# Kernel tuning notes

Hardware: AMD Instinct MI355X
Metric: run time of the kernel (lower is better)

Reference implementation:

```python
import jax, jax.numpy as jnp
import numpy as np

B, S = 512, 200            # batch, max_seq_len
D = H = 512                # embedding_dim must equal hidden_dim (ht init from embedded input)
VOCAB, USERS, SKILLS, OUT = 2002, 10000, 1001, 1001


def setup_inputs() -> dict:
    key = jax.random.key(0)
    ks = jax.random.split(key, 15)
    s = 0.05
    enc_emb = jax.random.normal(ks[0], (VOCAB, D)) * s
    enc_emb = enc_emb.at[0].set(0.0)  # padding_idx=0
    P = jax.random.normal(ks[1], (USERS, H)) * s
    Q = jax.random.normal(ks[2], (SKILLS, H)) * s
    P_bias = jax.random.normal(ks[3], (USERS, 1)) * s
    Q_bias = jax.random.normal(ks[4], (SKILLS, 1)) * s
    W_ih = jax.random.normal(ks[5], (4 * H, D)) * s   # torch LSTMCell weight_ih
    W_hh = jax.random.normal(ks[6], (4 * H, H)) * s   # torch LSTMCell weight_hh
    b_ih = jax.random.normal(ks[7], (4 * H,)) * s
    b_hh = jax.random.normal(ks[8], (4 * H,)) * s
    dec_W = jax.random.normal(ks[9], (OUT, H)) * s    # nn.Linear weight
    dec_b = jax.random.normal(ks[10], (OUT,)) * s
    main_input = jax.random.randint(ks[11], (B, S), 0, VOCAB)
    target_id = jax.random.randint(ks[12], (B, 1), 0, OUT)
    user_id_sequence = jax.random.randint(ks[13], (B, S), 0, USERS)
    skill_id_sequence = jax.random.randint(ks[14], (B, S), 0, SKILLS)
    return dict(main_input=main_input, target_id=target_id,
                user_id_sequence=user_id_sequence, skill_id_sequence=skill_id_sequence,
                enc_emb=enc_emb, P=P, Q=Q, P_bias=P_bias, Q_bias=Q_bias,
                W_ih=W_ih, W_hh=W_hh, b_ih=b_ih, b_hh=b_hh, dec_W=dec_W, dec_b=dec_b)


def reference(main_input, target_id, user_id_sequence, skill_id_sequence,
              enc_emb, P, Q, P_bias, Q_bias, W_ih, W_hh, b_ih, b_hh, dec_W, dec_b):
    x = enc_emb[main_input]                                    # [B,S,D] (dropout in eval mode = identity)
    # MF extended input: sigmoid(sum(P*Q, dim=2, keepdim) + P_bias + Q_bias) -> [B,S,1]
    mf = jax.nn.sigmoid(jnp.sum(P[user_id_sequence] * Q[skill_id_sequence], axis=2, keepdims=True)
                        + P_bias[user_id_sequence] + Q_bias[skill_id_sequence])

    def step(carry, inp):
        ht, ct = carry
        xt, et = inp                                           # xt:[B,D], et:[B,1]
        ct = ct + ct * et                                      # custom gating before cell update
        gates = xt @ W_ih.T + b_ih + ht @ W_hh.T + b_hh        # [B,4H], torch gate order i,f,g,o
        i, f, g, o = jnp.split(gates, 4, axis=-1)
        ct = jax.nn.sigmoid(f) * ct + jax.nn.sigmoid(i) * jnp.tanh(g)
        ht = jax.nn.sigmoid(o) * jnp.tanh(ct)
        return (ht, ct), None

    h0 = jnp.zeros((x.shape[0], H), x.dtype)
    (ht, _), _ = jax.lax.scan(step, (h0, h0),
                              (jnp.swapaxes(x, 0, 1), jnp.swapaxes(mf, 0, 1)))
    out = ht @ dec_W.T + dec_b                                 # [B,OUT]
    out = jnp.take_along_axis(out, target_id, axis=-1)         # [B,1]
    return jax.nn.sigmoid(out)
```

## Files before the change

kernel.cpp:

```cpp
#include <hip/hip_runtime.h>

typedef __attribute__((ext_vector_type(8))) short short8;
typedef __attribute__((ext_vector_type(4))) float floatx4;
typedef __attribute__((ext_vector_type(16))) float floatx16;
typedef unsigned int uint;
typedef unsigned short ushort;
typedef unsigned long long ull;
typedef __attribute__((ext_vector_type(4))) uint uintx4;
typedef __attribute__((ext_vector_type(4))) int intx4;

#define B_ 512
#define S_ 200
#define H_ 512
#define VOCAB_ 2002

__device__ __forceinline__ ushort f2bfbits(float f) {
  union { float f; uint u; } c; c.f = f;
  uint u = c.u;
  u += 0x7fffu + ((u >> 16) & 1u);
  return (ushort)(u >> 16);
}
__device__ __forceinline__ float bf2f_(ushort u) {
  union { uint i; float f; } c; c.i = ((uint)u) << 16; return c.f;
}
__device__ __forceinline__ float sigmoidf_(float x) { return 1.f / (1.f + __expf(-x)); }
__device__ __forceinline__ float tanhf_(float x) { return 2.f / (1.f + __expf(-2.f * x)) - 1.f; }
__device__ __forceinline__ float clamp30(float x) { return fminf(fmaxf(x, -30.f), 30.f); }

__device__ __forceinline__ void split8(const float* p, short8& hi, short8& lo) {
#pragma unroll
  for (int j = 0; j < 8; ++j) {
    const float f = p[j];
    const ushort h = f2bfbits(f);
    hi[j] = (short)h;
    lo[j] = (short)f2bfbits(f - bf2f_(h));
  }
}

__device__ __forceinline__ void ld16_cc(const void* p, uintx4& a) {
  asm volatile("global_load_dwordx4 %0, %1, off sc0 sc1"
               : "=&v"(a)
               : "v"(p));
}
__device__ __forceinline__ int ld4_cc_wait(const int* p) {
  int v;
  asm volatile("global_load_dword %0, %1, off sc0 sc1\n\t"
               "s_waitcnt vmcnt(0)"
               : "=v"(v)
               : "v"(p)
               : "memory");
  return v;
}
__device__ __forceinline__ void vm_wait0() {
  asm volatile("s_waitcnt vmcnt(0)" ::: "memory");
}
__device__ __forceinline__ void vm_wait4() {
  asm volatile("s_waitcnt vmcnt(4)" ::: "memory");
}

template <typename ET>
__global__ void encg_kernel(const float* __restrict__ emb, const float* __restrict__ Wih,
                            ET* __restrict__ encg) {
  const int w = threadIdx.x >> 6, l = threadIdx.x & 63;
  const int ln = l & 15, lk = l >> 4;
  const int n = (blockIdx.x * 4 + w) * 16 + ln;
  const int m = blockIdx.y * 16 + ln;
  const int mA = (m < VOCAB_) ? m : 0;
  const float* ap = emb + (size_t)mA * 512 + lk * 8;
  const float* bp = Wih + (size_t)n * 512 + lk * 8;
  floatx4 acc = {0.f, 0.f, 0.f, 0.f};
#pragma unroll 4
  for (int kk = 0; kk < 16; ++kk) {
    short8 ah, al, bh, bl;
    split8(ap + kk * 32, ah, al);
    split8(bp + kk * 32, bh, bl);
    acc = __builtin_amdgcn_mfma_f32_16x16x32_bf16(ah, bh, acc, 0, 0, 0);
    acc = __builtin_amdgcn_mfma_f32_16x16x32_bf16(ah, bl, acc, 0, 0, 0);
    acc = __builtin_amdgcn_mfma_f32_16x16x32_bf16(al, bh, acc, 0, 0, 0);
  }
#pragma unroll
  for (int r = 0; r < 4; ++r) {
    const int mo = blockIdx.y * 16 + lk * 4 + r;
    if (mo < VOCAB_) {
      if constexpr (sizeof(ET) == 2)
        encg[(size_t)mo * 2048 + n] = (ET)f2bfbits(acc[r]);
      else
        encg[(size_t)mo * 2048 + n] = acc[r];
    }
  }
}

__global__ void mf_kernel(const int* __restrict__ us, const int* __restrict__ ss,
                          const float* __restrict__ P, const float* __restrict__ Q,
                          const float* __restrict__ Pb, const float* __restrict__ Qb,
                          float* __restrict__ etb) {
  const int s = blockIdx.x;
  const int w = threadIdx.x >> 6, l = threadIdx.x & 63;
  const int b = blockIdx.y * 4 + w;
  const int u = us[b * S_ + s];
  const int k = ss[b * S_ + s];
  const float4 p0 = *(const float4*)(P + (size_t)u * 512 + l * 8);
  const float4 p1 = *(const float4*)(P + (size_t)u * 512 + l * 8 + 4);
  const float4 q0 = *(const float4*)(Q + (size_t)k * 512 + l * 8);
  const float4 q1 = *(const float4*)(Q + (size_t)k * 512 + l * 8 + 4);
  float dot = p0.x*q0.x + p0.y*q0.y + p0.z*q0.z + p0.w*q0.w
            + p1.x*q1.x + p1.y*q1.y + p1.z*q1.z + p1.w*q1.w;
#pragma unroll
  for (int off = 32; off > 0; off >>= 1) dot += __shfl_xor(dot, off);
  if (l == 0)
    etb[s * B_ + b] = sigmoidf_(dot + Pb[u] + Qb[k]);
}

template <typename ET>
__global__ __launch_bounds__(512, 2) void lstm_kernel(
    const int* __restrict__ tok, const ET* __restrict__ encg,
    const float* __restrict__ etb, const float* __restrict__ Whh,
    const float* __restrict__ bih, const float* __restrict__ bhh,
    ushort* ht_hi, ushort* ht_lo, int* ctr) {
  __shared__ __align__(16) ushort Ah_lds[32 * 512];
  __shared__ __align__(16) ushort Al_lds[32 * 512];
  __shared__ float gp_lds[2 * 128 * 33];

  const int bid = blockIdx.x;
  const int g = bid & 15, ns = bid >> 4;
  const int b0 = g * 32, h0 = ns * 32;
  const int tid = threadIdx.x;
  const int w = tid >> 6, l = tid & 63;
  const int nt = w & 3;
  const int kh = w >> 2;

  int* const myslot = ctr + g * 16 + ns;
  const int* const gslots = ctr + g * 16;

  short8 Bh[16], Bl[16];
  {
    const float* wr = Whh + (size_t)(nt * 512 + h0 + (l & 31)) * 512
                    + kh * 256 + (l >> 5) * 8;
#pragma unroll 4
    for (int kk = 0; kk < 16; ++kk)
      split8(wr + kk * 16, Bh[kk], Bl[kk]);
  }

  const int sr = tid >> 4;
  const int sc = tid & 15;
  const int hh = sc * 2;
  const int bg = b0 + sr;
  float ct0 = 0.f, ct1 = 0.f;

  float bs[4][2];
#pragma unroll
  for (int qq = 0; qq < 4; ++qq) {
    const int col = qq * 512 + h0 + hh;
    bs[qq][0] = bih[col] + bhh[col];
    bs[qq][1] = bih[col + 1] + bhh[col + 1];
  }

  const int swzw = (sr & 7) << 3;
  const int swzr = (l & 7) << 3;
  const int k8 = (l >> 5) * 8;
  const int sc8 = sc * 8;

  auto mfma_half = [&](int base) -> floatx16 {
    floatx16 a = {0.f,0.f,0.f,0.f,0.f,0.f,0.f,0.f,
                  0.f,0.f,0.f,0.f,0.f,0.f,0.f,0.f};
#pragma unroll
    for (int kk = 0; kk < 16; ++kk) {
      const int ao = (l & 31) * 512 + ((base + kk * 16 + k8) ^ swzr);
      const short8 ah = *(const short8*)(Ah_lds + ao);
      const short8 al = *(const short8*)(Al_lds + ao);
      a = __builtin_amdgcn_mfma_f32_32x32x16_bf16(ah, Bh[kk], a, 0, 0, 0);
      a = __builtin_amdgcn_mfma_f32_32x32x16_bf16(ah, Bl[kk], a, 0, 0, 0);
      a = __builtin_amdgcn_mfma_f32_32x32x16_bf16(al, Bh[kk], a, 0, 0, 0);
    }
    return a;
  };
  auto gp_write = [&](const floatx16& a) {
    float* gpw = gp_lds + kh * 4224 + (nt * 32 + (l & 31)) * 33 + 4 * (l >> 5);
#pragma unroll
    for (int r = 0; r < 16; ++r)
      gpw[(r & 3) + 8 * (r >> 2)] = a[r];
  };

  for (int s = 0; s < S_; ++s) {
    const int tv = tok[bg * S_ + s];
    float ev = etb[s * B_ + bg];
    float ex[4], ey[4];
#pragma unroll
    for (int qq = 0; qq < 4; ++qq) {
      if constexpr (sizeof(ET) == 2) {
        const uint e2 = *(const uint*)((const ushort*)encg + (size_t)tv * 2048 + qq * 512 + h0 + hh);
        ex[qq] = bf2f_((ushort)(e2 & 0xffffu)); ey[qq] = bf2f_((ushort)(e2 >> 16));
      } else {
        const float2 e = *(const float2*)((const float*)encg + (size_t)tv * 2048 + qq * 512 + h0 + hh);
        ex[qq] = e.x; ey[qq] = e.y;
      }
    }

    if (s > 0 && tid < 16) {
      const int* sp = gslots + tid;
      while (ld4_cc_wait(sp) < s) {}
    }
    __syncthreads();

    const size_t rdo = (size_t)(s & 1) * (B_ * H_);
    const size_t wro = (size_t)((s & 1) ^ 1) * (B_ * H_);
    const ushort* hrow = ht_hi + rdo + (size_t)bg * 512;
    const ushort* lrow = ht_lo + rdo + (size_t)bg * 512;

    uintx4 a0, a1, b0_, b1_;
    uintx4 a2, a3, b2_, b3_;
    __builtin_amdgcn_sched_barrier(0);
    ld16_cc(hrow + sc8,       a0);
    ld16_cc(hrow + sc8 + 128, a1);
    ld16_cc(lrow + sc8,       b0_);
    ld16_cc(lrow + sc8 + 128, b1_);
    ld16_cc(hrow + sc8 + 256, a2);
    ld16_cc(hrow + sc8 + 384, a3);
    ld16_cc(lrow + sc8 + 256, b2_);
    ld16_cc(lrow + sc8 + 384, b3_);
    vm_wait4();
    __builtin_amdgcn_sched_barrier(0);
    {
      const int base = sr * 512;
      *(uintx4*)(Ah_lds + base + (sc8 ^ swzw))         = a0;
      *(uintx4*)(Ah_lds + base + ((sc8 + 128) ^ swzw)) = a1;
      *(uintx4*)(Al_lds + base + (sc8 ^ swzw))         = b0_;
      *(uintx4*)(Al_lds + base + ((sc8 + 128) ^ swzw)) = b1_;
    }
    __syncthreads();

    floatx16 acc;
    if (kh == 0) {
      acc = mfma_half(0);
      gp_write(acc);
      vm_wait0();
      __builtin_amdgcn_sched_barrier(0);
      const int base = sr * 512;
      *(uintx4*)(Ah_lds + base + ((sc8 + 256) ^ swzw)) = a2;
      *(uintx4*)(Ah_lds + base + ((sc8 + 384) ^ swzw)) = a3;
      *(uintx4*)(Al_lds + base + ((sc8 + 256) ^ swzw)) = b2_;
      *(uintx4*)(Al_lds + base + ((sc8 + 384) ^ swzw)) = b3_;
    } else {
      vm_wait0();
      __builtin_amdgcn_sched_barrier(0);
      const int base = sr * 512;
      *(uintx4*)(Ah_lds + base + ((sc8 + 256) ^ swzw)) = a2;
      *(uintx4*)(Ah_lds + base + ((sc8 + 384) ^ swzw)) = a3;
      *(uintx4*)(Al_lds + base + ((sc8 + 256) ^ swzw)) = b2_;
      *(uintx4*)(Al_lds + base + ((sc8 + 384) ^ swzw)) = b3_;
    }
    __syncthreads();

    if (kh == 1) {
      acc = mfma_half(256);
      gp_write(acc);
    }
    __syncthreads();

    {
      ev = fminf(fmaxf(ev, 0.f), 1.f);
      float Gv[4][2];
#pragma unroll
      for (int qq = 0; qq < 4; ++qq) {
        const int cb0 = (qq * 32 + hh) * 33 + sr;
        const int cb1 = (qq * 32 + hh + 1) * 33 + sr;
        Gv[qq][0] = clamp30(gp_lds[cb0] + gp_lds[4224 + cb0] + ex[qq] + bs[qq][0]);
        Gv[qq][1] = clamp30(gp_lds[cb1] + gp_lds[4224 + cb1] + ey[qq] + bs[qq][1]);
      }
      const float scale = 1.f + ev;
      float c0v = ct0 * scale;
      c0v = sigmoidf_(Gv[1][0]) * c0v + sigmoidf_(Gv[0][0]) * tanhf_(Gv[2][0]);
      const float h0v = sigmoidf_(Gv[3][0]) * tanhf_(c0v);
      ct0 = c0v;
      float c1v = ct1 * scale;
      c1v = sigmoidf_(Gv[1][1]) * c1v + sigmoidf_(Gv[0][1]) * tanhf_(Gv[2][1]);
      const float h1v = sigmoidf_(Gv[3][1]) * tanhf_(c1v);
      ct1 = c1v;
      const ushort h0h = f2bfbits(h0v), h1h = f2bfbits(h1v);
      const ushort h0l = f2bfbits(h0v - bf2f_(h0h)), h1l = f2bfbits(h1v - bf2f_(h1h));
      const size_t wo = wro + (size_t)bg * 512 + h0 + hh;
      __hip_atomic_store((uint*)(ht_hi + wo), (uint)h0h | ((uint)h1h << 16),
                         __ATOMIC_RELAXED, __HIP_MEMORY_SCOPE_AGENT);
      __hip_atomic_store((uint*)(ht_lo + wo), (uint)h0l | ((uint)h1l << 16),
                         __ATOMIC_RELAXED, __HIP_MEMORY_SCOPE_AGENT);
    }

    vm_wait0();
    __syncthreads();
    if (tid == 0)
      __hip_atomic_store(myslot, s + 1, __ATOMIC_RELAXED, __HIP_MEMORY_SCOPE_AGENT);
  }
}

__global__ void dec_kernel(const ushort* __restrict__ hthi, const ushort* __restrict__ htlo,
                           const float* __restrict__ decW, const float* __restrict__ decb,
                           const int* __restrict__ tgt, float* __restrict__ out) {
  const int w = threadIdx.x >> 6, l = threadIdx.x & 63;
  const int b = blockIdx.x * 4 + w;
  const int t = tgt[b];
  const uint4 hv = *(const uint4*)(hthi + (size_t)b * 512 + l * 8);
  const uint4 lv = *(const uint4*)(htlo + (size_t)b * 512 + l * 8);
  const float4 w0 = *(const float4*)(decW + (size_t)t * 512 + l * 8);
  const float4 w1 = *(const float4*)(decW + (size_t)t * 512 + l * 8 + 4);
  const uint ha[4] = {hv.x, hv.y, hv.z, hv.w};
  const uint la[4] = {lv.x, lv.y, lv.z, lv.w};
  float hf[8];
#pragma unroll
  for (int i = 0; i < 4; ++i) {
    hf[2*i]   = bf2f_((ushort)(ha[i] & 0xffffu)) + bf2f_((ushort)(la[i] & 0xffffu));
    hf[2*i+1] = bf2f_((ushort)(ha[i] >> 16))     + bf2f_((ushort)(la[i] >> 16));
  }
  float dot = hf[0]*w0.x + hf[1]*w0.y + hf[2]*w0.z + hf[3]*w0.w
            + hf[4]*w1.x + hf[5]*w1.y + hf[6]*w1.z + hf[7]*w1.w;
#pragma unroll
  for (int off = 32; off > 0; off >>= 1) dot += __shfl_xor(dot, off);
  if (l == 0) out[b] = sigmoidf_(dot + decb[t]);
}

extern "C" void kernel_launch(void* const* d_in, const int* in_sizes, int n_in,
                              void* d_out, int out_size, void* d_ws, size_t ws_size,
                              hipStream_t stream) {
  (void)in_sizes; (void)n_in; (void)out_size;
  const int* main_input = (const int*)d_in[0];
  const int* target_id  = (const int*)d_in[1];
  const int* user_seq   = (const int*)d_in[2];
  const int* skill_seq  = (const int*)d_in[3];
  const float* enc_emb  = (const float*)d_in[4];
  const float* P        = (const float*)d_in[5];
  const float* Q        = (const float*)d_in[6];
  const float* Pb       = (const float*)d_in[7];
  const float* Qb       = (const float*)d_in[8];
  const float* W_ih     = (const float*)d_in[9];
  const float* W_hh     = (const float*)d_in[10];
  const float* b_ih     = (const float*)d_in[11];
  const float* b_hh     = (const float*)d_in[12];
  const float* dec_W    = (const float*)d_in[13];
  const float* dec_b    = (const float*)d_in[14];
  float* out = (float*)d_out;

  char* wsb = (char*)d_ws;
  ushort* ht_hi = (ushort*)wsb;
  ushort* ht_lo = (ushort*)(wsb + 1048576);
  int* ctr = (int*)(wsb + 2097152);
  float* etb = (float*)(wsb + 2113536);
  char* encb = wsb + 2523136;
  const bool enc32 = ws_size >= (size_t)2523136 + 16400384;

  hipMemsetAsync(wsb, 0, 2113536, stream);

  if (enc32)
    encg_kernel<float><<<dim3(32, 126), dim3(256), 0, stream>>>(enc_emb, W_ih, (float*)encb);
  else
    encg_kernel<ushort><<<dim3(32, 126), dim3(256), 0, stream>>>(enc_emb, W_ih, (ushort*)encb);
  mf_kernel<<<dim3(200, 128), dim3(256), 0, stream>>>(user_seq, skill_seq, P, Q, Pb, Qb, etb);
  if (enc32)
    lstm_kernel<float><<<dim3(256), dim3(512), 0, stream>>>(
        main_input, (const float*)encb, etb, W_hh, b_ih, b_hh, ht_hi, ht_lo, ctr);
  else
    lstm_kernel<ushort><<<dim3(256), dim3(512), 0, stream>>>(
        main_input, (const ushort*)encb, etb, W_hh, b_ih, b_hh, ht_hi, ht_lo, ctr);
  dec_kernel<<<dim3(128), dim3(256), 0, stream>>>(ht_hi, ht_lo, dec_W, dec_b, target_id, out);
}
```

Measured before the change: 2.673 ms.

## Split h-tile staging per K-half with LDS counter sync instead of barriers

```diff
diff --git a/kernel.cpp b/kernel.cpp
--- a/kernel.cpp
+++ b/kernel.cpp
@@ -7,7 +7,6 @@
 typedef unsigned short ushort;
 typedef unsigned long long ull;
 typedef __attribute__((ext_vector_type(4))) uint uintx4;
-typedef __attribute__((ext_vector_type(4))) int intx4;
 
 #define B_ 512
 #define S_ 200
@@ -53,9 +52,6 @@
 }
 __device__ __forceinline__ void vm_wait0() {
   asm volatile("s_waitcnt vmcnt(0)" ::: "memory");
-}
-__device__ __forceinline__ void vm_wait4() {
-  asm volatile("s_waitcnt vmcnt(4)" ::: "memory");
 }
 
 template <typename ET>
@@ -120,6 +116,7 @@
   __shared__ __align__(16) ushort Ah_lds[32 * 512];
   __shared__ __align__(16) ushort Al_lds[32 * 512];
   __shared__ float gp_lds[2 * 128 * 33];
+  __shared__ int cnt[2];
 
   const int bid = blockIdx.x;
   const int g = bid & 15, ns = bid >> 4;
@@ -155,10 +152,16 @@
     bs[qq][1] = bih[col + 1] + bhh[col + 1];
   }
 
-  const int swzw = (sr & 7) << 3;
+  const int srs = (tid & 255) >> 3;
+  const int cs = tid & 7;
+  const int colb = kh * 256 + cs * 8;
+  const int bgs = b0 + srs;
+  const int swzw = (srs & 7) << 3;
   const int swzr = (l & 7) << 3;
   const int k8 = (l >> 5) * 8;
-  const int sc8 = sc * 8;
+
+  if (tid == 0) { cnt[0] = 0; cnt[1] = 0; }
+  __syncthreads();
 
   auto mfma_half = [&](int base) -> floatx16 {
     floatx16 a = {0.f,0.f,0.f,0.f,0.f,0.f,0.f,0.f,
@@ -196,65 +199,46 @@
       }
     }
 
-    if (s > 0 && tid < 16) {
-      const int* sp = gslots + tid;
+    if (s > 0 && l < 8) {
+      const int* sp = gslots + kh * 8 + l;
       while (ld4_cc_wait(sp) < s) {}
     }
-    __syncthreads();
 
     const size_t rdo = (size_t)(s & 1) * (B_ * H_);
     const size_t wro = (size_t)((s & 1) ^ 1) * (B_ * H_);
-    const ushort* hrow = ht_hi + rdo + (size_t)bg * 512;
-    const ushort* lrow = ht_lo + rdo + (size_t)bg * 512;
-
-    uintx4 a0, a1, b0_, b1_;
-    uintx4 a2, a3, b2_, b3_;
-    __builtin_amdgcn_sched_barrier(0);
-    ld16_cc(hrow + sc8,       a0);
-    ld16_cc(hrow + sc8 + 128, a1);
-    ld16_cc(lrow + sc8,       b0_);
-    ld16_cc(lrow + sc8 + 128, b1_);
-    ld16_cc(hrow + sc8 + 256, a2);
-    ld16_cc(hrow + sc8 + 384, a3);
-    ld16_cc(lrow + sc8 + 256, b2_);
-    ld16_cc(lrow + sc8 + 384, b3_);
-    vm_wait4();
-    __builtin_amdgcn_sched_barrier(0);
+
     {
-      const int base = sr * 512;
-      *(uintx4*)(Ah_lds + base + (sc8 ^ swzw))         = a0;
-      *(uintx4*)(Ah_lds + base + ((sc8 + 128) ^ swzw)) = a1;
-      *(uintx4*)(Al_lds + base + (sc8 ^ swzw))         = b0_;
-      *(uintx4*)(Al_lds + base + ((sc8 + 128) ^ swzw)) = b1_;
-    }
-    __syncthreads();
-
-    floatx16 acc;
-    if (kh == 0) {
-      acc = mfma_half(0);
-      gp_write(acc);
+      const ushort* hrow = ht_hi + rdo + (size_t)bgs * 512;
+      const ushort* lrow = ht_lo + rdo + (size_t)bgs * 512;
+      uintx4 a0, a1, a2, a3, c0, c1, c2, c3;
+      ld16_cc(hrow + colb,       a0);
+      ld16_cc(hrow + colb + 64,  a1);
+      ld16_cc(hrow + colb + 128, a2);
+      ld16_cc(hrow + colb + 192, a3);
+      ld16_cc(lrow + colb,       c0);
+      ld16_cc(lrow + colb + 64,  c1);
+      ld16_cc(lrow + colb + 128, c2);
+      ld16_cc(lrow + colb + 192, c3);
       vm_wait0();
       __builtin_amdgcn_sched_barrier(0);
-      const int base = sr * 512;
-      *(uintx4*)(Ah_lds + base + ((sc8 + 256) ^ swzw)) = a2;
-      *(uintx4*)(Ah_lds + base + ((sc8 + 384) ^ swzw)) = a3;
-      *(uintx4*)(Al_lds + base + ((sc8 + 256) ^ swzw)) = b2_;
-      *(uintx4*)(Al_lds + base + ((sc8 + 384) ^ swzw)) = b3_;
-    } else {
-      vm_wait0();
-      __builtin_amdgcn_sched_barrier(0);
-      const int base = sr * 512;
-      *(uintx4*)(Ah_lds + base + ((sc8 + 256) ^ swzw)) = a2;
-      *(uintx4*)(Ah_lds + base + ((sc8 + 384) ^ swzw)) = a3;
-      *(uintx4*)(Al_lds + base + ((sc8 + 256) ^ swzw)) = b2_;
-      *(uintx4*)(Al_lds + base + ((sc8 + 384) ^ swzw)) = b3_;
-    }
-    __syncthreads();
-
-    if (kh == 1) {
-      acc = mfma_half(256);
-      gp_write(acc);
-    }
+      const int base = srs * 512;
+      *(uintx4*)(Ah_lds + base + ((colb)       ^ swzw)) = a0;
+      *(uintx4*)(Ah_lds + base + ((colb + 64)  ^ swzw)) = a1;
+      *(uintx4*)(Ah_lds + base + ((colb + 128) ^ swzw)) = a2;
+      *(uintx4*)(Ah_lds + base + ((colb + 192) ^ swzw)) = a3;
+      *(uintx4*)(Al_lds + base + ((colb)       ^ swzw)) = c0;
+      *(uintx4*)(Al_lds + base + ((colb + 64)  ^ swzw)) = c1;
+      *(uintx4*)(Al_lds + base + ((colb + 128) ^ swzw)) = c2;
+      *(uintx4*)(Al_lds + base + ((colb + 192) ^ swzw)) = c3;
+    }
+    if (l == 0)
+      __hip_atomic_fetch_add(&cnt[kh], 1, __ATOMIC_RELEASE, __HIP_MEMORY_SCOPE_WORKGROUP);
+    while (__hip_atomic_load(&cnt[kh], __ATOMIC_ACQUIRE, __HIP_MEMORY_SCOPE_WORKGROUP)
+           < 4 * (s + 1)) {}
+    __builtin_amdgcn_sched_barrier(0);
+
+    floatx16 acc = mfma_half(kh * 256);
+    gp_write(acc);
     __syncthreads();
 
     {
```

Result: slower. 2.849 ms (+6.6%).
